# Kernel tuning notes

Measured on AMD Instinct MI355X. Metric: run time of the kernel, lower is better.

Reference implementation:

```python
import jax, jax.numpy as jnp
import numpy as np

NUM_INPUTS = 1024
NUM_HIDDEN = 1024
FORGET_GATE_BIAS = -1.0
EPS = 1e-5


def layer_norm_1d(x, weight, bias):
    # Matches torch LayerNorm1D: std is unbiased (ddof=1), divide by (std + eps)
    mean = jnp.mean(x, axis=1, keepdims=True)
    std = jnp.std(x, axis=1, keepdims=True, ddof=1)
    return (x - mean) / (std + EPS) * weight + bias


def setup_inputs() -> dict:
    key = jax.random.key(0)
    ks = jax.random.split(key, 8)
    B, I, H = 4096, NUM_INPUTS, NUM_HIDDEN
    lim_i = 1.0 / np.sqrt(I)
    lim_h = 1.0 / np.sqrt(H)
    return {
        "inputs": jax.random.normal(ks[0], (B, I), jnp.float32),
        "hx": jax.random.normal(ks[1], (B, H), jnp.float32),
        "cx": jax.random.normal(ks[2], (B, H), jnp.float32),
        "w_i2h": jax.random.uniform(ks[3], (4 * H, I), jnp.float32, -lim_i, lim_i),
        "b_i2h": jax.random.uniform(ks[4], (4 * H,), jnp.float32, -lim_i, lim_i),
        "w_h2h": jax.random.uniform(ks[5], (4 * H, H), jnp.float32, -lim_h, lim_h),
        "b_h2h": jax.random.uniform(ks[6], (4 * H,), jnp.float32, -lim_h, lim_h),
        "ln_i2h_w": jnp.ones((1, 4 * H), jnp.float32),
        "ln_i2h_b": jnp.zeros((1, 4 * H), jnp.float32),
        "ln_h2h_w": jnp.ones((1, 4 * H), jnp.float32),
        "ln_h2h_b": jnp.zeros((1, 4 * H), jnp.float32),
        "ln_h2o_w": jnp.ones((1, H), jnp.float32),
        "ln_h2o_b": jnp.zeros((1, H), jnp.float32),
    }


def reference(inputs, hx, cx, w_i2h, b_i2h, w_h2h, b_h2h,
              ln_i2h_w, ln_i2h_b, ln_h2h_w, ln_h2h_b, ln_h2o_w, ln_h2o_b):
    H = NUM_HIDDEN
    i2h = inputs @ w_i2h.T + b_i2h          # [B, 4H]
    h2h = hx @ w_h2h.T + b_h2h              # [B, 4H]
    x = layer_norm_1d(i2h, ln_i2h_w, ln_i2h_b) + layer_norm_1d(h2h, ln_h2h_w, ln_h2h_b)
    g_i, g_f, g_o, g_c = jnp.split(x, 4, axis=1)
    in_gate = jax.nn.sigmoid(g_i)
    forget_gate = jax.nn.sigmoid(g_f + FORGET_GATE_BIAS)
    out_gate = jax.nn.sigmoid(g_o)
    in_transform = jnp.tanh(g_c)
    cx_new = forget_gate * cx + in_gate * in_transform
    hx_new = out_gate * jnp.tanh(layer_norm_1d(cx_new, ln_h2o_w, ln_h2o_b))
    return hx_new, cx_new
```

## Files before the change

kernel.cpp:

```cpp
#include <hip/hip_runtime.h>
#include <hip/hip_bf16.h>
#include <math.h>

#define NI 1024
#define NH 1024
#define H4 4096
#define FGB (-1.0f)
#define LN_EPS 1e-5f
#define NKT 32

typedef unsigned short u16;
typedef __attribute__((ext_vector_type(8))) short short8;
typedef __attribute__((ext_vector_type(8))) unsigned short ushort8v;
typedef __attribute__((ext_vector_type(16))) float f32x16;

__device__ __forceinline__ float bf2f(u16 u) {
    union { unsigned int i; float f; } v; v.i = ((unsigned int)u) << 16; return v.f;
}
__device__ __forceinline__ u16 f2bf(float f) {
    __hip_bfloat16 h = __float2bfloat16(f);
    return __builtin_bit_cast(u16, h);
}
__device__ __forceinline__ ushort8v cvt8(float4 lo, float4 hi) {
    ushort8v r;
    r[0] = f2bf(lo.x); r[1] = f2bf(lo.y); r[2] = f2bf(lo.z); r[3] = f2bf(lo.w);
    r[4] = f2bf(hi.x); r[5] = f2bf(hi.y); r[6] = f2bf(hi.z); r[7] = f2bf(hi.w);
    return r;
}
__device__ __forceinline__ float fast_sigmoid(float x) {
    return 1.0f / (1.0f + __expf(-x));
}
__device__ __forceinline__ float fast_tanh(float x) {
    return 1.0f - 2.0f / (__expf(2.0f * x) + 1.0f);
}

__device__ __forceinline__ void gload16(const u16* g, u16* l) {
    __builtin_amdgcn_global_load_lds(
        (const __attribute__((address_space(1))) void*)g,
        (__attribute__((address_space(3))) void*)l,
        16, 0, 0);
}

__global__ __launch_bounds__(256) void shuffle_cast(
    const float* __restrict__ a, const float* __restrict__ b,
    const float* __restrict__ c, const float* __restrict__ d,
    u16* __restrict__ oa, u16* __restrict__ ob,
    u16* __restrict__ oc, u16* __restrict__ od)
{
    const int my = blockIdx.y;
    const float* src = (my == 0) ? a : (my == 1) ? b : (my == 2) ? c : d;
    u16*         dst = (my == 0) ? oa : (my == 1) ? ob : (my == 2) ? oc : od;

    const int lane = threadIdx.x & 63;
    const int wave = threadIdx.x >> 6;
    const int p    = blockIdx.x * 4 + wave;
    const int mtile = p >> 5;
    const int kt    = p & 31;

    const int row  = mtile * 32 + (lane & 31);
    const int colf = kt * 32 + (lane >> 5) * 8;
    const float* s = src + (size_t)row * 1024 + colf;
    u16* o = dst + (size_t)p * 1024 + lane * 8;

    float4 l0 = *(const float4*)(s);
    float4 h0 = *(const float4*)(s + 4);
    float4 l1 = *(const float4*)(s + 16);
    float4 h1 = *(const float4*)(s + 20);
    *(ushort8v*)(o)       = cvt8(l0, h0);
    *(ushort8v*)(o + 512) = cvt8(l1, h1);
}

__global__ __launch_bounds__(512, 2) void gemm_lds(
    const u16* __restrict__ Af0, const u16* __restrict__ Wf0,
    const float* __restrict__ bias0, u16* __restrict__ C0,
    const u16* __restrict__ Af1, const u16* __restrict__ Wf1,
    const float* __restrict__ bias1, u16* __restrict__ C1,
    int N)
{
    const u16*   Af   = blockIdx.z ? Af1 : Af0;
    const u16*   Wf   = blockIdx.z ? Wf1 : Wf0;
    const float* bias = blockIdx.z ? bias1 : bias0;
    u16*         C    = blockIdx.z ? C1 : C0;

    __shared__ __align__(16) u16 sA[4][8][2][512];
    __shared__ __align__(16) u16 sB[4][8][2][512];

    const int tid  = threadIdx.x;
    const int lane = tid & 63;
    const int wave = tid >> 6;
    const int wm   = wave >> 2;
    const int wn   = wave & 3;

    const u16* gA = Af + (size_t)(blockIdx.y * 8 + wave) * 32768 + lane * 8;
    const u16* gB = Wf + (size_t)(blockIdx.x * 8 + wave) * 32768 + lane * 8;

    f32x16 acc[4][2];
#pragma unroll
    for (int i = 0; i < 4; ++i)
#pragma unroll
        for (int j = 0; j < 2; ++j)
#pragma unroll
            for (int r = 0; r < 16; ++r)
                acc[i][j][r] = 0.f;

#define STAGE_A(kt)                                                          \
    do {                                                                     \
        gload16(gA + (size_t)(kt) * 1024,       &sA[(kt) & 3][wave][0][0]);  \
        gload16(gA + (size_t)(kt) * 1024 + 512, &sA[(kt) & 3][wave][1][0]);  \
    } while (0)
#define STAGE_B(kt)                                                          \
    do {                                                                     \
        gload16(gB + (size_t)(kt) * 1024,       &sB[(kt) & 3][wave][0][0]);  \
        gload16(gB + (size_t)(kt) * 1024 + 512, &sB[(kt) & 3][wave][1][0]);  \
    } while (0)

#define LDFRAGS(kh)                                                          \
    do {                                                                     \
        a0 = *(const ushort8v*)&sA[slot][wm * 4 + 0][kh][lane * 8];          \
        a1 = *(const ushort8v*)&sA[slot][wm * 4 + 1][kh][lane * 8];          \
        a2 = *(const ushort8v*)&sA[slot][wm * 4 + 2][kh][lane * 8];          \
        a3 = *(const ushort8v*)&sA[slot][wn == wn ? wm * 4 + 3 : 0][kh][lane * 8]; \
    } while (0)

#define MFMA8()                                                                                      \
    do {                                                                                             \
        acc[0][0] = __builtin_amdgcn_mfma_f32_32x32x16_bf16((short8)a0, (short8)b0, acc[0][0], 0, 0, 0); \
        acc[1][0] = __builtin_amdgcn_mfma_f32_32x32x16_bf16((short8)a1, (short8)b0, acc[1][0], 0, 0, 0); \
        acc[2][0] = __builtin_amdgcn_mfma_f32_32x32x16_bf16((short8)a2, (short8)b0, acc[2][0], 0, 0, 0); \
        acc[3][0] = __builtin_amdgcn_mfma_f32_32x32x16_bf16((short8)a3, (short8)b0, acc[3][0], 0, 0, 0); \
        acc[0][1] = __builtin_amdgcn_mfma_f32_32x32x16_bf16((short8)a0, (short8)b1, acc[0][1], 0, 0, 0); \
        acc[1][1] = __builtin_amdgcn_mfma_f32_32x32x16_bf16((short8)a1, (short8)b1, acc[1][1], 0, 0, 0); \
        acc[2][1] = __builtin_amdgcn_mfma_f32_32x32x16_bf16((short8)a2, (short8)b1, acc[2][1], 0, 0, 0); \
        acc[3][1] = __builtin_amdgcn_mfma_f32_32x32x16_bf16((short8)a3, (short8)b1, acc[3][1], 0, 0, 0); \
    } while (0)

    STAGE_A(0); STAGE_B(0);
    STAGE_A(1); STAGE_B(1);
    STAGE_A(2); STAGE_B(2);

    asm volatile("s_waitcnt vmcnt(8)" ::: "memory");
    __builtin_amdgcn_s_barrier();

    ushort8v a0, a1, a2, a3, b0, b1;

    for (int kt = 0; kt < NKT; ++kt) {
        const int slot = kt & 3;

        a0 = *(const ushort8v*)&sA[slot][wm * 4 + 0][0][lane * 8];
        a1 = *(const ushort8v*)&sA[slot][wm * 4 + 1][0][lane * 8];
        a2 = *(const ushort8v*)&sA[slot][wm * 4 + 2][0][lane * 8];
        a3 = *(const ushort8v*)&sA[slot][wm * 4 + 3][0][lane * 8];
        b0 = *(const ushort8v*)&sB[slot][wn * 2 + 0][0][lane * 8];
        b1 = *(const ushort8v*)&sB[slot][wn * 2 + 1][0][lane * 8];
        if (kt + 3 < NKT) STAGE_A(kt + 3);
        __builtin_amdgcn_s_barrier();
        asm volatile("s_waitcnt lgkmcnt(0)" ::: "memory");
        __builtin_amdgcn_s_setprio(1);
        MFMA8();
        __builtin_amdgcn_s_setprio(0);
        __builtin_amdgcn_s_barrier();

        a0 = *(const ushort8v*)&sA[slot][wm * 4 + 0][1][lane * 8];
        a1 = *(const ushort8v*)&sA[slot][wm * 4 + 1][1][lane * 8];
        a2 = *(const ushort8v*)&sA[slot][wm * 4 + 2][1][lane * 8];
        a3 = *(const ushort8v*)&sA[slot][wm * 4 + 3][1][lane * 8];
        b0 = *(const ushort8v*)&sB[slot][wn * 2 + 0][1][lane * 8];
        b1 = *(const ushort8v*)&sB[slot][wn * 2 + 1][1][lane * 8];
        if (kt + 3 < NKT) STAGE_B(kt + 3);
        __builtin_amdgcn_s_barrier();
        asm volatile("s_waitcnt lgkmcnt(0)" ::: "memory");
        __builtin_amdgcn_s_setprio(1);
        MFMA8();
        __builtin_amdgcn_s_setprio(0);
        if (kt < NKT - 3) {
            asm volatile("s_waitcnt vmcnt(8)" ::: "memory");
        } else if (kt == NKT - 3) {
            asm volatile("s_waitcnt vmcnt(4)" ::: "memory");
        } else if (kt == NKT - 2) {
            asm volatile("s_waitcnt vmcnt(0)" ::: "memory");
        }
        __builtin_amdgcn_s_barrier();
    }
#undef STAGE_A
#undef STAGE_B
#undef LDFRAGS
#undef MFMA8

    const int m0  = blockIdx.y * 256;
    const int n0  = blockIdx.x * 256;
    const int l31 = lane & 31;
    float bv[2];
#pragma unroll
    for (int tn = 0; tn < 2; ++tn)
        bv[tn] = bias[n0 + wn * 64 + tn * 32 + l31];

    const int rbase = (lane >> 5) * 4;
#pragma unroll
    for (int tm = 0; tm < 4; ++tm)
#pragma unroll
        for (int reg = 0; reg < 16; ++reg) {
            const int row = m0 + wm * 128 + tm * 32 + (reg & 3) + 8 * (reg >> 2) + rbase;
#pragma unroll
            for (int tn = 0; tn < 2; ++tn) {
                const int col = n0 + wn * 64 + tn * 32 + l31;
                C[(size_t)row * N + col] = f2bf(acc[tm][tn][reg] + bv[tn]);
            }
        }
}

__global__ __launch_bounds__(256) void lstm_pointwise(
    const u16* __restrict__ i2h, const u16* __restrict__ h2h,
    const float* __restrict__ cx,
    const float* __restrict__ lwx, const float* __restrict__ lbx,
    const float* __restrict__ lwy, const float* __restrict__ lby,
    const float* __restrict__ lwc, const float* __restrict__ lbc,
    float* __restrict__ hx_out, float* __restrict__ cx_out)
{
    __shared__ u16 sX[H4];
    __shared__ u16 sY[H4];
    __shared__ float red[16];

    const int row  = blockIdx.x;
    const int tid  = threadIdx.x;
    const int lane = tid & 63;
    const int wid  = tid >> 6;

    const u16* xr = i2h + (size_t)row * H4;
    const u16* yr = h2h + (size_t)row * H4;

    float sx = 0.f, sxx = 0.f, sy = 0.f, syy = 0.f;
#pragma unroll
    for (int s = 0; s < 2; ++s) {
        const int off = s * 2048 + tid * 8;
        ushort8v xv = *(const ushort8v*)(xr + off);
        ushort8v yv = *(const ushort8v*)(yr + off);
        *(ushort8v*)(sX + off) = xv;
        *(ushort8v*)(sY + off) = yv;
#pragma unroll
        for (int e = 0; e < 8; ++e) {
            float x = bf2f(xv[e]), y = bf2f(yv[e]);
            sx += x; sxx += x * x; sy += y; syy += y * y;
        }
    }
#pragma unroll
    for (int m = 32; m; m >>= 1) {
        sx  += __shfl_xor(sx,  m, 64);
        sxx += __shfl_xor(sxx, m, 64);
        sy  += __shfl_xor(sy,  m, 64);
        syy += __shfl_xor(syy, m, 64);
    }
    if (lane == 0) {
        red[wid] = sx; red[4 + wid] = sxx; red[8 + wid] = sy; red[12 + wid] = syy;
    }
    __syncthreads();
    const float tsx  = red[0] + red[1] + red[2] + red[3];
    const float tsxx = red[4] + red[5] + red[6] + red[7];
    const float tsy  = red[8] + red[9] + red[10] + red[11];
    const float tsyy = red[12] + red[13] + red[14] + red[15];
    __syncthreads();

    const float n1  = (float)H4;
    const float mx  = tsx / n1;
    const float ivx = 1.0f / (sqrtf(fmaxf((tsxx - tsx * tsx / n1) / (n1 - 1.f), 0.f)) + LN_EPS);
    const float my  = tsy / n1;
    const float ivy = 1.0f / (sqrtf(fmaxf((tsyy - tsy * tsy / n1) / (n1 - 1.f), 0.f)) + LN_EPS);

    const int j0 = tid * 4;
    float gate[4][4];
#pragma unroll
    for (int g = 0; g < 4; ++g) {
        ushort4 xv = *(const ushort4*)(sX + g * NH + j0);
        ushort4 yv = *(const ushort4*)(sY + g * NH + j0);
        float4 wxv = *(const float4*)(lwx + g * NH + j0);
        float4 bxv = *(const float4*)(lbx + g * NH + j0);
        float4 wyv = *(const float4*)(lwy + g * NH + j0);
        float4 byv = *(const float4*)(lby + g * NH + j0);
        gate[g][0] = (bf2f(xv.x) - mx) * ivx * wxv.x + bxv.x + (bf2f(yv.x) - my) * ivy * wyv.x + byv.x;
        gate[g][1] = (bf2f(xv.y) - mx) * ivx * wxv.y + bxv.y + (bf2f(yv.y) - my) * ivy * wyv.y + byv.y;
        gate[g][2] = (bf2f(xv.z) - mx) * ivx * wxv.z + bxv.z + (bf2f(yv.z) - my) * ivy * wyv.z + byv.z;
        gate[g][3] = (bf2f(xv.w) - mx) * ivx * wxv.w + bxv.w + (bf2f(yv.w) - my) * ivy * wyv.w + byv.w;
    }

    float4 cxv = *(const float4*)(cx + (size_t)row * NH + j0);
    const float cin[4] = {cxv.x, cxv.y, cxv.z, cxv.w};
    float cvl[4], og[4];
    float sc = 0.f, scc = 0.f;
#pragma unroll
    for (int e = 0; e < 4; ++e) {
        float ing = fast_sigmoid(gate[0][e]);
        float fg  = fast_sigmoid(gate[1][e] + FGB);
        og[e]     = fast_sigmoid(gate[2][e]);
        float tr  = fast_tanh(gate[3][e]);
        float c   = fg * cin[e] + ing * tr;
        cvl[e] = c; sc += c; scc += c * c;
    }
    *(float4*)(cx_out + (size_t)row * NH + j0) = make_float4(cvl[0], cvl[1], cvl[2], cvl[3]);

#pragma unroll
    for (int m = 32; m; m >>= 1) {
        sc  += __shfl_xor(sc,  m, 64);
        scc += __shfl_xor(scc, m, 64);
    }
    if (lane == 0) { red[wid] = sc; red[4 + wid] = scc; }
    __syncthreads();
    const float tsc  = red[0] + red[1] + red[2] + red[3];
    const float tscc = red[4] + red[5] + red[6] + red[7];

    const float nc  = (float)NH;
    const float mc  = tsc / nc;
    const float ivc = 1.0f / (sqrtf(fmaxf((tscc - tsc * tsc / nc) / (nc - 1.f), 0.f)) + LN_EPS);

    float4 wcv = *(const float4*)(lwc + j0);
    float4 bcv = *(const float4*)(lbc + j0);
    float h0 = og[0] * fast_tanh((cvl[0] - mc) * ivc * wcv.x + bcv.x);
    float h1 = og[1] * fast_tanh((cvl[1] - mc) * ivc * wcv.y + bcv.y);
    float h2 = og[2] * fast_tanh((cvl[2] - mc) * ivc * wcv.z + bcv.z);
    float h3 = og[3] * fast_tanh((cvl[3] - mc) * ivc * wcv.w + bcv.w);
    *(float4*)(hx_out + (size_t)row * NH + j0) = make_float4(h0, h1, h2, h3);
}

extern "C" void kernel_launch(void* const* d_in, const int* in_sizes, int n_in,
                              void* d_out, int out_size, void* d_ws, size_t ws_size,
                              hipStream_t stream) {
    const float* inputs = (const float*)d_in[0];
    const float* hx     = (const float*)d_in[1];
    const float* cx     = (const float*)d_in[2];
    const float* w_i2h  = (const float*)d_in[3];
    const float* b_i2h  = (const float*)d_in[4];
    const float* w_h2h  = (const float*)d_in[5];
    const float* b_h2h  = (const float*)d_in[6];
    const float* lwx    = (const float*)d_in[7];
    const float* lbx    = (const float*)d_in[8];
    const float* lwy    = (const float*)d_in[9];
    const float* lby    = (const float*)d_in[10];
    const float* lwc    = (const float*)d_in[11];
    const float* lbc    = (const float*)d_in[12];

    const int B = in_sizes[0] / NI;

    u16* a_fr   = (u16*)d_ws;
    u16* hx_fr  = a_fr   + (size_t)B * NI;
    u16* wi_fr  = hx_fr  + (size_t)B * NH;
    u16* wh_fr  = wi_fr  + (size_t)H4 * NI;
    u16* i2h_bf = wh_fr  + (size_t)H4 * NH;
    u16* h2h_bf = i2h_bf + (size_t)B * H4;

    float* hx_out = (float*)d_out;
    float* cx_out = hx_out + (size_t)B * NH;

    shuffle_cast<<<dim3(1024, 4), dim3(256), 0, stream>>>(
        inputs, hx, w_i2h, w_h2h, a_fr, hx_fr, wi_fr, wh_fr);

    gemm_lds<<<dim3(H4 / 256, B / 256, 2), dim3(512), 0, stream>>>(
        a_fr, wi_fr, b_i2h, i2h_bf,
        hx_fr, wh_fr, b_h2h, h2h_bf,
        H4);

    lstm_pointwise<<<dim3(B), dim3(256), 0, stream>>>(
        i2h_bf, h2h_bf, cx, lwx, lbx, lwy, lby, lwc, lbc, hx_out, cx_out);
}
```

Before: 243.8 us.

## Restructure GEMM K-loop to one barrier per tile and coalesce cast kernel via LDS

The GEMM main loop is rewritten so each K tile issues both A and B prefetches after a single waitcnt+barrier, reads all twelve fragments up front, and runs sixteen MFMAs. This replaces the previous three barriers per tile and the split half-tile structure, and the loop is unrolled by four with constant LDS slots. The shuffle/cast kernel now reads fully coalesced rows into an LDS tile before writing the fragment layout, using half as many blocks. Register pressure rises from holding twice as many fragments at once. Moving the single barrier ahead of the prefetch also changes ordering between the LDS slot being overwritten and the other waves' reads of it.

```diff
diff --git a/kernel.cpp b/kernel.cpp
--- a/kernel.cpp
+++ b/kernel.cpp
@@ -21,12 +21,6 @@
     __hip_bfloat16 h = __float2bfloat16(f);
     return __builtin_bit_cast(u16, h);
 }
-__device__ __forceinline__ ushort8v cvt8(float4 lo, float4 hi) {
-    ushort8v r;
-    r[0] = f2bf(lo.x); r[1] = f2bf(lo.y); r[2] = f2bf(lo.z); r[3] = f2bf(lo.w);
-    r[4] = f2bf(hi.x); r[5] = f2bf(hi.y); r[6] = f2bf(hi.z); r[7] = f2bf(hi.w);
-    return r;
-}
 __device__ __forceinline__ float fast_sigmoid(float x) {
     return 1.0f / (1.0f + __expf(-x));
 }
@@ -47,27 +41,42 @@
     u16* __restrict__ oa, u16* __restrict__ ob,
     u16* __restrict__ oc, u16* __restrict__ od)
 {
+    __shared__ u16 sT[32][264];
+
     const int my = blockIdx.y;
     const float* src = (my == 0) ? a : (my == 1) ? b : (my == 2) ? c : d;
     u16*         dst = (my == 0) ? oa : (my == 1) ? ob : (my == 2) ? oc : od;
 
-    const int lane = threadIdx.x & 63;
-    const int wave = threadIdx.x >> 6;
-    const int p    = blockIdx.x * 4 + wave;
-    const int mtile = p >> 5;
-    const int kt    = p & 31;
-
-    const int row  = mtile * 32 + (lane & 31);
-    const int colf = kt * 32 + (lane >> 5) * 8;
-    const float* s = src + (size_t)row * 1024 + colf;
-    u16* o = dst + (size_t)p * 1024 + lane * 8;
-
-    float4 l0 = *(const float4*)(s);
-    float4 h0 = *(const float4*)(s + 4);
-    float4 l1 = *(const float4*)(s + 16);
-    float4 h1 = *(const float4*)(s + 20);
-    *(ushort8v*)(o)       = cvt8(l0, h0);
-    *(ushort8v*)(o + 512) = cvt8(l1, h1);
+    const int mtile = blockIdx.x >> 2;
+    const int slab  = blockIdx.x & 3;
+    const int t     = threadIdx.x;
+    const int w     = t >> 6;
+    const int lane  = t & 63;
+
+    const float* s0 = src + (size_t)(mtile * 32) * 1024 + slab * 256 + lane * 4;
+#pragma unroll
+    for (int i = 0; i < 8; ++i) {
+        const int row = i * 4 + w;
+        float4 v = *(const float4*)(s0 + (size_t)row * 1024);
+        ushort4 pk;
+        pk.x = f2bf(v.x); pk.y = f2bf(v.y); pk.z = f2bf(v.z); pk.w = f2bf(v.w);
+        *(ushort4*)&sT[row][lane * 4] = pk;
+    }
+    __syncthreads();
+
+    const int r  = lane & 31;
+    const int hi = lane >> 5;
+#pragma unroll
+    for (int j = 0; j < 2; ++j) {
+        const int ktl = w * 2 + j;
+        const int kt  = slab * 8 + ktl;
+        u16* o = dst + ((size_t)(mtile * 32 + kt)) * 1024 + lane * 8;
+#pragma unroll
+        for (int kh = 0; kh < 2; ++kh) {
+            ushort8v vv = *(const ushort8v*)&sT[r][ktl * 32 + kh * 16 + hi * 8];
+            *(ushort8v*)(o + kh * 512) = vv;
+        }
+    }
 }
 
 __global__ __launch_bounds__(512, 2) void gemm_lds(
@@ -114,77 +123,78 @@
         gload16(gB + (size_t)(kt) * 1024 + 512, &sB[(kt) & 3][wave][1][0]);  \
     } while (0)
 
-#define LDFRAGS(kh)                                                          \
+    ushort8v a00, a10, a20, a30, a01, a11, a21, a31;
+    ushort8v b00, b10, b01, b11;
+
+#define READS(slot)                                                          \
     do {                                                                     \
-        a0 = *(const ushort8v*)&sA[slot][wm * 4 + 0][kh][lane * 8];          \
-        a1 = *(const ushort8v*)&sA[slot][wm * 4 + 1][kh][lane * 8];          \
-        a2 = *(const ushort8v*)&sA[slot][wm * 4 + 2][kh][lane * 8];          \
-        a3 = *(const ushort8v*)&sA[slot][wn == wn ? wm * 4 + 3 : 0][kh][lane * 8]; \
-    } while (0)
-
-#define MFMA8()                                                                                      \
-    do {                                                                                             \
-        acc[0][0] = __builtin_amdgcn_mfma_f32_32x32x16_bf16((short8)a0, (short8)b0, acc[0][0], 0, 0, 0); \
-        acc[1][0] = __builtin_amdgcn_mfma_f32_32x32x16_bf16((short8)a1, (short8)b0, acc[1][0], 0, 0, 0); \
-        acc[2][0] = __builtin_amdgcn_mfma_f32_32x32x16_bf16((short8)a2, (short8)b0, acc[2][0], 0, 0, 0); \
-        acc[3][0] = __builtin_amdgcn_mfma_f32_32x32x16_bf16((short8)a3, (short8)b0, acc[3][0], 0, 0, 0); \
-        acc[0][1] = __builtin_amdgcn_mfma_f32_32x32x16_bf16((short8)a0, (short8)b1, acc[0][1], 0, 0, 0); \
-        acc[1][1] = __builtin_amdgcn_mfma_f32_32x32x16_bf16((short8)a1, (short8)b1, acc[1][1], 0, 0, 0); \
-        acc[2][1] = __builtin_amdgcn_mfma_f32_32x32x16_bf16((short8)a2, (short8)b1, acc[2][1], 0, 0, 0); \
-        acc[3][1] = __builtin_amdgcn_mfma_f32_32x32x16_bf16((short8)a3, (short8)b1, acc[3][1], 0, 0, 0); \
+        a00 = *(const ushort8v*)&sA[slot][wm * 4 + 0][0][lane * 8];          \
+        b00 = *(const ushort8v*)&sB[slot][wn * 2 + 0][0][lane * 8];          \
+        a10 = *(const ushort8v*)&sA[slot][wm * 4 + 1][0][lane * 8];          \
+        b10 = *(const ushort8v*)&sB[slot][wn * 2 + 1][0][lane * 8];          \
+        a20 = *(const ushort8v*)&sA[slot][wm * 4 + 2][0][lane * 8];          \
+        a30 = *(const ushort8v*)&sA[slot][wm * 4 + 3][0][lane * 8];          \
+        a01 = *(const ushort8v*)&sA[slot][wm * 4 + 0][1][lane * 8];          \
+        b01 = *(const ushort8v*)&sB[slot][wn * 2 + 0][1][lane * 8];          \
+        a11 = *(const ushort8v*)&sA[slot][wm * 4 + 1][1][lane * 8];          \
+        b11 = *(const ushort8v*)&sB[slot][wn * 2 + 1][1][lane * 8];          \
+        a21 = *(const ushort8v*)&sA[slot][wm * 4 + 2][1][lane * 8];          \
+        a31 = *(const ushort8v*)&sA[slot][wm * 4 + 3][1][lane * 8];          \
+    } while (0)
+
+#define MFMAS()                                                                                        \
+    do {                                                                                               \
+        acc[0][0] = __builtin_amdgcn_mfma_f32_32x32x16_bf16((short8)a00, (short8)b00, acc[0][0], 0, 0, 0); \
+        acc[1][0] = __builtin_amdgcn_mfma_f32_32x32x16_bf16((short8)a10, (short8)b00, acc[1][0], 0, 0, 0); \
+        acc[0][1] = __builtin_amdgcn_mfma_f32_32x32x16_bf16((short8)a00, (short8)b10, acc[0][1], 0, 0, 0); \
+        acc[1][1] = __builtin_amdgcn_mfma_f32_32x32x16_bf16((short8)a10, (short8)b10, acc[1][1], 0, 0, 0); \
+        acc[2][0] = __builtin_amdgcn_mfma_f32_32x32x16_bf16((short8)a20, (short8)b00, acc[2][0], 0, 0, 0); \
+        acc[3][0] = __builtin_amdgcn_mfma_f32_32x32x16_bf16((short8)a30, (short8)b00, acc[3][0], 0, 0, 0); \
+        acc[2][1] = __builtin_amdgcn_mfma_f32_32x32x16_bf16((short8)a20, (short8)b10, acc[2][1], 0, 0, 0); \
+        acc[3][1] = __builtin_amdgcn_mfma_f32_32x32x16_bf16((short8)a30, (short8)b10, acc[3][1], 0, 0, 0); \
+        acc[0][0] = __builtin_amdgcn_mfma_f32_32x32x16_bf16((short8)a01, (short8)b01, acc[0][0], 0, 0, 0); \
+        acc[1][0] = __builtin_amdgcn_mfma_f32_32x32x16_bf16((short8)a11, (short8)b01, acc[1][0], 0, 0, 0); \
+        acc[0][1] = __builtin_amdgcn_mfma_f32_32x32x16_bf16((short8)a01, (short8)b11, acc[0][1], 0, 0, 0); \
+        acc[1][1] = __builtin_amdgcn_mfma_f32_32x32x16_bf16((short8)a11, (short8)b11, acc[1][1], 0, 0, 0); \
+        acc[2][0] = __builtin_amdgcn_mfma_f32_32x32x16_bf16((short8)a21, (short8)b01, acc[2][0], 0, 0, 0); \
+        acc[3][0] = __builtin_amdgcn_mfma_f32_32x32x16_bf16((short8)a31, (short8)b01, acc[3][0], 0, 0, 0); \
+        acc[2][1] = __builtin_amdgcn_mfma_f32_32x32x16_bf16((short8)a21, (short8)b11, acc[2][1], 0, 0, 0); \
+        acc[3][1] = __builtin_amdgcn_mfma_f32_32x32x16_bf16((short8)a31, (short8)b11, acc[3][1], 0, 0, 0); \
+    } while (0)
+
+#define KT_STEP(kt, slot, VM, DO_STAGE)                                      \
+    do {                                                                     \
+        asm volatile("s_waitcnt vmcnt(" VM ")" ::: "memory");                \
+        __builtin_amdgcn_s_barrier();                                        \
+        asm volatile("" ::: "memory");                                       \
+        if (DO_STAGE) { STAGE_A((kt) + 3); STAGE_B((kt) + 3); }              \
+        READS(slot);                                                         \
+        __builtin_amdgcn_s_setprio(1);                                       \
+        MFMAS();                                                             \
+        __builtin_amdgcn_s_setprio(0);                                       \
     } while (0)
 
     STAGE_A(0); STAGE_B(0);
     STAGE_A(1); STAGE_B(1);
     STAGE_A(2); STAGE_B(2);
 
-    asm volatile("s_waitcnt vmcnt(8)" ::: "memory");
-    __builtin_amdgcn_s_barrier();
-
-    ushort8v a0, a1, a2, a3, b0, b1;
-
-    for (int kt = 0; kt < NKT; ++kt) {
-        const int slot = kt & 3;
-
-        a0 = *(const ushort8v*)&sA[slot][wm * 4 + 0][0][lane * 8];
-        a1 = *(const ushort8v*)&sA[slot][wm * 4 + 1][0][lane * 8];
-        a2 = *(const ushort8v*)&sA[slot][wm * 4 + 2][0][lane * 8];
-        a3 = *(const ushort8v*)&sA[slot][wm * 4 + 3][0][lane * 8];
-        b0 = *(const ushort8v*)&sB[slot][wn * 2 + 0][0][lane * 8];
-        b1 = *(const ushort8v*)&sB[slot][wn * 2 + 1][0][lane * 8];
-        if (kt + 3 < NKT) STAGE_A(kt + 3);
-        __builtin_amdgcn_s_barrier();
-        asm volatile("s_waitcnt lgkmcnt(0)" ::: "memory");
-        __builtin_amdgcn_s_setprio(1);
-        MFMA8();
-        __builtin_amdgcn_s_setprio(0);
-        __builtin_amdgcn_s_barrier();
-
-        a0 = *(const ushort8v*)&sA[slot][wm * 4 + 0][1][lane * 8];
-        a1 = *(const ushort8v*)&sA[slot][wm * 4 + 1][1][lane * 8];
-        a2 = *(const ushort8v*)&sA[slot][wm * 4 + 2][1][lane * 8];
-        a3 = *(const ushort8v*)&sA[slot][wm * 4 + 3][1][lane * 8];
-        b0 = *(const ushort8v*)&sB[slot][wn * 2 + 0][1][lane * 8];
-        b1 = *(const ushort8v*)&sB[slot][wn * 2 + 1][1][lane * 8];
-        if (kt + 3 < NKT) STAGE_B(kt + 3);
-        __builtin_amdgcn_s_barrier();
-        asm volatile("s_waitcnt lgkmcnt(0)" ::: "memory");
-        __builtin_amdgcn_s_setprio(1);
-        MFMA8();
-        __builtin_amdgcn_s_setprio(0);
-        if (kt < NKT - 3) {
-            asm volatile("s_waitcnt vmcnt(8)" ::: "memory");
-        } else if (kt == NKT - 3) {
-            asm volatile("s_waitcnt vmcnt(4)" ::: "memory");
-        } else if (kt == NKT - 2) {
-            asm volatile("s_waitcnt vmcnt(0)" ::: "memory");
-        }
-        __builtin_amdgcn_s_barrier();
-    }
+#pragma unroll
+    for (int kt = 0; kt < NKT - 4; kt += 4) {
+        KT_STEP(kt + 0, 0, "8", true);
+        KT_STEP(kt + 1, 1, "8", true);
+        KT_STEP(kt + 2, 2, "8", true);
+        KT_STEP(kt + 3, 3, "8", true);
+    }
+    KT_STEP(NKT - 4, 0, "8", true);
+    KT_STEP(NKT - 3, 1, "8", false);
+    KT_STEP(NKT - 2, 2, "4", false);
+    KT_STEP(NKT - 1, 3, "0", false);
+
 #undef STAGE_A
 #undef STAGE_B
-#undef LDFRAGS
-#undef MFMA8
+#undef READS
+#undef MFMAS
+#undef KT_STEP
 
     const int m0  = blockIdx.y * 256;
     const int n0  = blockIdx.x * 256;
@@ -348,7 +358,7 @@
     float* hx_out = (float*)d_out;
     float* cx_out = hx_out + (size_t)B * NH;
 
-    shuffle_cast<<<dim3(1024, 4), dim3(256), 0, stream>>>(
+    shuffle_cast<<<dim3(512, 4), dim3(256), 0, stream>>>(
         inputs, hx, w_i2h, w_h2h, a_fr, hx_fr, wi_fr, wh_fr);
 
     gemm_lds<<<dim3(H4 / 256, B / 256, 2), dim3(512), 0, stream>>>(
```

Result: no change. 243.9 us (+0.0%).
